# Optimization experiments

Hardware: AMD Instinct MI355X
Metric: run time of the kernel (lower is better)

## Reference

```python
import jax, jax.numpy as jnp
import numpy as np
from jax import lax

SUB_NO = 20; T_NO = 200; BASIS_NO = 19; T_DATA = 100000; E_NO = 800; I_NO = 200


def make_cos_basis():
    # raised-cosine log-time basis, [BASIS_NO, T_NO]
    i = jnp.arange(BASIS_NO, dtype=jnp.float32)[:, None]
    phi = (jnp.pi / 2.0) * i
    x = jnp.arange(T_NO, dtype=jnp.float32)[None, :]
    raw = 5.0 * jnp.log(x + 1.0)  # cos_scale=5, cos_shift=1
    basis = 0.5 * jnp.cos(raw - phi) + 0.5
    return jnp.where((raw >= phi - jnp.pi) & (raw <= phi + jnp.pi), basis, 0.0)


def causal_group_conv(x, kern):
    # x: [T, sub], kern: [sub, T_no]; out[t,k] = sum_j kern[k,j]*x[t-j,k]
    xr = x.T[None]  # [1, sub, T]
    w = jnp.flip(kern, 1)[:, None, :]  # [sub, 1, T_no]
    out = lax.conv_general_dilated(xr, w, (1,), [(T_NO - 1, 0)],
                                   dimension_numbers=('NCH', 'OIH', 'NCH'),
                                   feature_group_count=kern.shape[0])
    return out[0].T  # [T, sub]


def hist_conv(z, kern):
    # matches torch: pad T_no leading zeros, valid corr with flipped kernel, drop last
    zp = jnp.concatenate([jnp.zeros((T_NO,), z.dtype), z])[None, None, :]
    w = jnp.flip(kern)[None, None, :]
    out = lax.conv_general_dilated(zp, w, (1,), 'VALID',
                                   dimension_numbers=('NCH', 'OIH', 'NCH'))
    return out[0, 0, :-1]  # [T]


def setup_inputs() -> dict:
    key = jax.random.key(0)
    ks = jax.random.split(key, 12)
    # binary dendritic tree: parent of node j is (j-1)//2; C_den[p, j] = 1
    parent = np.maximum((np.arange(SUB_NO) - 1) // 2, 0)
    C_den = np.zeros((SUB_NO, SUB_NO), np.float32)
    for j in range(1, SUB_NO):
        C_den[parent[j], j] = 1.0
    assign_e = jax.random.randint(ks[0], (E_NO,), 0, SUB_NO)
    assign_i = jax.random.randint(ks[1], (I_NO,), 0, SUB_NO)
    C_syn_e = jax.nn.one_hot(assign_e, SUB_NO, dtype=jnp.float32).T
    C_syn_i = jax.nn.one_hot(assign_i, SUB_NO, dtype=jnp.float32).T
    S_e = (jax.random.uniform(ks[2], (T_DATA, E_NO)) < 0.05).astype(jnp.float32)
    S_i = (jax.random.uniform(ks[3], (T_DATA, I_NO)) < 0.05).astype(jnp.float32)
    Z = (jax.random.uniform(ks[4], (T_DATA,)) < 0.02).astype(jnp.float32)
    return {
        'S_e': S_e, 'S_i': S_i, 'Z': Z,
        'C_den': jnp.asarray(C_den), 'C_syn_e': C_syn_e, 'C_syn_i': C_syn_i,
        'W_syn_ns': 0.1 * jax.random.normal(ks[5], (SUB_NO, BASIS_NO, 2)),
        'W_syn_s': 0.1 * jax.random.normal(ks[6], (SUB_NO, BASIS_NO, 2)),
        'W_sub_ns': 0.1 * jnp.ones((SUB_NO,), jnp.float32),
        'W_sub_s': 0.1 * jnp.ones((SUB_NO,), jnp.float32),
        'V_o': jax.random.normal(ks[7], (1,)),
        'Theta_ns': 0.1 * jax.random.normal(ks[8], (SUB_NO,)),
        'Theta_s': 0.1 * jax.random.normal(ks[9], (SUB_NO,)),
        'hist_s_weights': 0.1 * jax.random.normal(ks[10], (BASIS_NO,)),
        'hist_ns_weights': 0.1 * jax.random.normal(ks[11], (BASIS_NO,)),
    }


def reference(S_e, S_i, Z, C_den, C_syn_e, C_syn_i, W_syn_ns, W_syn_s,
              W_sub_ns, W_sub_s, V_o, Theta_ns, Theta_s,
              hist_s_weights, hist_ns_weights):
    cb = make_cos_basis()
    syn_e = S_e @ C_syn_e.T  # [T, sub]
    syn_i = S_i @ C_syn_i.T
    e_kern_ns = W_syn_ns[:, :, 0] @ cb  # [sub, T_no]
    i_kern_ns = W_syn_ns[:, :, 1] @ cb
    e_kern_s = W_syn_s[:, :, 0] @ cb
    i_kern_s = W_syn_s[:, :, 1] @ cb
    syn_ns = causal_group_conv(syn_e, e_kern_ns) + causal_group_conv(syn_i, i_kern_ns)
    syn_s = causal_group_conv(syn_e, e_kern_s) + causal_group_conv(syn_i, i_kern_s)
    ws2 = W_sub_s ** 2
    wns2 = W_sub_ns ** 2
    T = S_e.shape[0]
    s_out = jnp.zeros((T, SUB_NO), syn_s.dtype)
    ns_out = jnp.zeros((T, SUB_NO), syn_ns.dtype)
    # leaf-to-root tree message passing; C_den[k] masks children of node k
    for k in range(SUB_NO - 1, 0, -1):
        mask = C_den[k]
        s_out = s_out.at[:, k].set(jnp.tanh(syn_s[:, k] + s_out @ (mask * ws2) + Theta_s[k]))
        ns_out = ns_out.at[:, k].set(jnp.tanh(syn_ns[:, k] + ns_out @ (mask * wns2) + Theta_ns[k]))
    hist_s_kern = hist_s_weights @ cb  # [T_no]
    hist_ns_kern = hist_ns_weights @ cb
    root_mask = C_den[0]
    final_Z = jax.nn.sigmoid(hist_conv(Z, hist_s_kern) + syn_s[:, 0]
                             + s_out @ (root_mask * ws2) + Theta_s[0])
    root_ns = jnp.tanh(hist_conv(Z, hist_ns_kern) + syn_ns[:, 0]
                       + ns_out @ (root_mask * wns2) + Theta_ns[0])
    final_V = root_ns * wns2[0] + V_o[0]
    out_filters = jnp.vstack([e_kern_ns, i_kern_ns, e_kern_s, i_kern_s,
                              hist_ns_kern[None], hist_s_kern[None]])
    return final_V, final_Z, out_filters
```

## Files before the change

### kernel.cpp

```cpp
#include <hip/hip_runtime.h>
#include <hip/hip_bf16.h>
#include <math.h>

#define SUB_NO 20
#define T_NO   200
#define BASIS_NO 19
#define T_DATA 100000
#define E_NO   800
#define I_NO   200

using u16 = unsigned short;
using u32 = unsigned int;
using u64 = unsigned long long;

__device__ __forceinline__ float bf2f(u16 h) {
  return __builtin_bit_cast(float, (u32)h << 16);
}
__device__ __forceinline__ u16 f2bf(float f) {
  u32 u = __builtin_bit_cast(u32, f);
  u += 0x7FFFu + ((u >> 16) & 1u);
  return (u16)(u >> 16);
}
__device__ __forceinline__ float ldx(const void* p, int i, bool bf) {
  return bf ? bf2f(((const u16*)p)[i]) : ((const float*)p)[i];
}
__device__ __forceinline__ void stx(void* p, int i, float v, bool bf) {
  if (bf) ((u16*)p)[i] = f2bf(v); else ((float*)p)[i] = v;
}

#define K0_BLOCKS 21
__global__ __launch_bounds__(256) void k0_prep(
    const u32* __restrict__ probe,
    const void* __restrict__ Wns, const void* __restrict__ Ws,
    const void* __restrict__ hsw, const void* __restrict__ hnsw,
    const void* __restrict__ Cse, const void* __restrict__ Csi,
    float* __restrict__ kern4, float* __restrict__ hist_s,
    float* __restrict__ hist_ns, int* __restrict__ ae, int* __restrict__ ai,
    void* __restrict__ out) {
  const bool bf = (probe[0] != 0u);
  __shared__ float cb[BASIS_NO * T_NO];
  const int tid = threadIdx.x;
  constexpr float PI = 3.14159265358979323846f;
  for (int idx = tid; idx < BASIS_NO * T_NO; idx += 256) {
    int b = idx / T_NO, j = idx - b * T_NO;
    float phi = 0.5f * PI * (float)b;
    float raw = 5.0f * logf((float)j + 1.0f);
    float v = 0.f;
    if (raw >= phi - PI && raw <= phi + PI) v = 0.5f * cosf(raw - phi) + 0.5f;
    cb[idx] = v;
  }
  __syncthreads();
  const int fbase = 2 * T_DATA;
  for (int gid = blockIdx.x * 256 + tid; gid < 5200; gid += K0_BLOCKS * 256) {
    if (gid < 4000) {
      int k = gid / T_NO, j = gid - k * T_NO;
      float e_ns = 0.f, i_ns = 0.f, e_s = 0.f, i_s = 0.f;
#pragma unroll
      for (int b = 0; b < BASIS_NO; ++b) {
        float c = cb[b * T_NO + j];
        e_ns = fmaf(ldx(Wns, (k * BASIS_NO + b) * 2 + 0, bf), c, e_ns);
        i_ns = fmaf(ldx(Wns, (k * BASIS_NO + b) * 2 + 1, bf), c, i_ns);
        e_s  = fmaf(ldx(Ws,  (k * BASIS_NO + b) * 2 + 0, bf), c, e_s);
        i_s  = fmaf(ldx(Ws,  (k * BASIS_NO + b) * 2 + 1, bf), c, i_s);
      }
      float* kp = kern4 + (j * SUB_NO + k) * 4;
      kp[0] = e_ns; kp[1] = i_ns; kp[2] = e_s; kp[3] = i_s;
      stx(out, fbase + (0 * SUB_NO + k) * T_NO + j, e_ns, bf);
      stx(out, fbase + (1 * SUB_NO + k) * T_NO + j, i_ns, bf);
      stx(out, fbase + (2 * SUB_NO + k) * T_NO + j, e_s,  bf);
      stx(out, fbase + (3 * SUB_NO + k) * T_NO + j, i_s,  bf);
    } else if (gid < 4200) {
      int j = gid - 4000;
      float hs = 0.f, hns = 0.f;
#pragma unroll
      for (int b = 0; b < BASIS_NO; ++b) {
        float c = cb[b * T_NO + j];
        hs  = fmaf(ldx(hsw,  b, bf), c, hs);
        hns = fmaf(ldx(hnsw, b, bf), c, hns);
      }
      hist_s[j] = hs; hist_ns[j] = hns;
      stx(out, fbase + 80 * T_NO + j, hns, bf);
      stx(out, fbase + 81 * T_NO + j, hs,  bf);
    } else if (gid < 5000) {
      int e = gid - 4200;
      int a = 0;
      for (int k = 0; k < SUB_NO; ++k) if (ldx(Cse, k * E_NO + e, bf) != 0.f) a = k;
      ae[e] = a;
    } else {
      int e = gid - 5000;
      int a = 0;
      for (int k = 0; k < SUB_NO; ++k) if (ldx(Csi, k * I_NO + e, bf) != 0.f) a = k;
      ai[e] = a;
    }
  }
}

#define K1_R 128

__global__ __launch_bounds__(256) void k1_agg(
    const u32* __restrict__ probe,
    const void* __restrict__ Se, const void* __restrict__ Si,
    const int* __restrict__ ae, const int* __restrict__ ai,
    u32* __restrict__ syn_pair) {
  const bool bf = (probe[0] != 0u);
  __shared__ u64 mask_e[SUB_NO][16];
  __shared__ u64 mask_i[SUB_NO][8];
  __shared__ int lae[E_NO];
  __shared__ int lai[I_NO];
  const int tid = threadIdx.x;
  const int l = tid & 63;
  const int wv = tid >> 6;
  for (int n = tid; n < E_NO; n += 256) lae[n] = ae[n];
  for (int n = tid; n < I_NO; n += 256) lai[n] = ai[n];
  __syncthreads();
  for (int pid = tid; pid < 480; pid += 256) {
    if (pid < 320) {
      int k = pid >> 4, w = pid & 15;
      u64 m = 0;
      if (bf) {
        if (w < 8) { for (int b = 0; b < 64; ++b) if (lae[8 * b + w] == k) m |= 1ull << b; }
        else       { for (int b = 0; b < 36; ++b) if (lae[512 + 8 * b + (w - 8)] == k) m |= 1ull << b; }
      } else {
        int g = w >> 2, j = w & 3;
        int lim = (g < 3) ? 64 : 8;
        for (int b = 0; b < lim; ++b) if (lae[256 * g + 4 * b + j] == k) m |= 1ull << b;
      }
      mask_e[k][w] = m;
    } else {
      int p2 = pid - 320; int k = p2 >> 3, w = p2 & 7;
      u64 m = 0;
      if (bf) { for (int b = 0; b < 25; ++b) { int e = 8 * b + w; if (e < I_NO && lai[e] == k) m |= 1ull << b; } }
      else if (w < 4) { for (int b = 0; b < 50; ++b) if (lai[4 * b + w] == k) m |= 1ull << b; }
      mask_i[k][w] = m;
    }
  }
  __syncthreads();
  u64 rme[16], rmi[8];
  const int ke = (l < SUB_NO) ? l : 0;
  const int ki = (l >= 32 && l < 32 + SUB_NO) ? l - 32 : 0;
#pragma unroll
  for (int w = 0; w < 16; ++w) rme[w] = mask_e[ke][w];
#pragma unroll
  for (int w = 0; w < 8; ++w) rmi[w] = mask_i[ki][w];

  const int r0 = blockIdx.x * K1_R + wv * 32;
  int nrows = T_DATA - r0; if (nrows > 32) nrows = 32;
  if (nrows <= 0) return;
  const uint4 z4 = make_uint4(0u, 0u, 0u, 0u);

  if (bf) {
    uint4 a0, a1, c0;
    {
      const uint4* p = (const uint4*)((const u16*)Se + (size_t)r0 * E_NO);
      a0 = p[l]; a1 = (l < 36) ? p[64 + l] : z4;
      const uint4* pi = (const uint4*)((const u16*)Si + (size_t)r0 * I_NO);
      c0 = (l < 25) ? pi[l] : z4;
    }
    for (int i = 0; i < nrows; ++i) {
      const int t = r0 + i;
      uint4 b0 = z4, b1 = z4, d0 = z4;
      if (i + 1 < nrows) {
        const uint4* p = (const uint4*)((const u16*)Se + (size_t)(t + 1) * E_NO);
        b0 = p[l]; b1 = (l < 36) ? p[64 + l] : z4;
        const uint4* pi = (const uint4*)((const u16*)Si + (size_t)(t + 1) * I_NO);
        d0 = (l < 25) ? pi[l] : z4;
      }
      u32 ce = 0, ci = 0;
#pragma unroll
      for (int j = 0; j < 8; ++j) {
        u32 d = (&a0.x)[j >> 1];
        u32 h = (j & 1) ? (d >> 16) : (d & 0xFFFFu);
        u64 m = __ballot(h != 0u);
        ce += (u32)__popcll(rme[j] & m);
      }
#pragma unroll
      for (int j = 0; j < 8; ++j) {
        u32 d = (&a1.x)[j >> 1];
        u32 h = (j & 1) ? (d >> 16) : (d & 0xFFFFu);
        u64 m = __ballot(h != 0u);
        ce += (u32)__popcll(rme[8 + j] & m);
      }
#pragma unroll
      for (int j = 0; j < 8; ++j) {
        u32 d = (&c0.x)[j >> 1];
        u32 h = (j & 1) ? (d >> 16) : (d & 0xFFFFu);
        u64 m = __ballot(h != 0u);
        ci += (u32)__popcll(rmi[j] & m);
      }
      u32 pe = (u32)f2bf((float)ce);
      u32 pif = (u32)f2bf((float)ci);
      u32 other = __shfl(pif, (l + 32) & 63, 64);
      if (l < SUB_NO) syn_pair[(size_t)t * SUB_NO + l] = pe | (other << 16);
      a0 = b0; a1 = b1; c0 = d0;
    }
  } else {
    uint4 a0, a1, a2, a3, c0;
    {
      const uint4* p = (const uint4*)((const float*)Se + (size_t)r0 * E_NO);
      a0 = p[l]; a1 = p[64 + l]; a2 = p[128 + l]; a3 = (l < 8) ? p[192 + l] : z4;
      const uint4* pi = (const uint4*)((const float*)Si + (size_t)r0 * I_NO);
      c0 = (l < 50) ? pi[l] : z4;
    }
    for (int i = 0; i < nrows; ++i) {
      const int t = r0 + i;
      uint4 b0 = z4, b1 = z4, b2 = z4, b3 = z4, d0 = z4;
      if (i + 1 < nrows) {
        const uint4* p = (const uint4*)((const float*)Se + (size_t)(t + 1) * E_NO);
        b0 = p[l]; b1 = p[64 + l]; b2 = p[128 + l]; b3 = (l < 8) ? p[192 + l] : z4;
        const uint4* pi = (const uint4*)((const float*)Si + (size_t)(t + 1) * I_NO);
        d0 = (l < 50) ? pi[l] : z4;
      }
      u32 ce = 0, ci = 0;
      const uint4 va[4] = {a0, a1, a2, a3};
#pragma unroll
      for (int g = 0; g < 4; ++g) {
#pragma unroll
        for (int j = 0; j < 4; ++j) {
          u32 d = (&va[g].x)[j];
          u64 m = __ballot(d != 0u);
          ce += (u32)__popcll(rme[4 * g + j] & m);
        }
      }
#pragma unroll
      for (int j = 0; j < 4; ++j) {
        u32 d = (&c0.x)[j];
        u64 m = __ballot(d != 0u);
        ci += (u32)__popcll(rmi[j] & m);
      }
      u32 pe = (u32)f2bf((float)ce);
      u32 pif = (u32)f2bf((float)ci);
      u32 other = __shfl(pif, (l + 32) & 63, 64);
      if (l < SUB_NO) syn_pair[(size_t)t * SUB_NO + l] = pe | (other << 16);
      a0 = b0; a1 = b1; a2 = b2; a3 = b3; c0 = d0;
    }
  }
}

#define K2T  64
#define K2R  (K2T + T_NO)
#define K2CH 40

__global__ __launch_bounds__(320) void k2_conv(
    const u32* __restrict__ probe,
    const u32* __restrict__ syn_pair, const float* __restrict__ kern4,
    const float* __restrict__ hist_s, const float* __restrict__ hist_ns,
    const void* __restrict__ Z, const void* __restrict__ Wsub_ns,
    const void* __restrict__ Wsub_s, const void* __restrict__ Vo,
    const void* __restrict__ Thns, const void* __restrict__ Ths,
    void* __restrict__ out) {
  const bool bf = (probe[0] != 0u);
  __shared__ uint4 tile4[K2R * 5];
  __shared__ float4 kc4[K2CH * SUB_NO];
  __shared__ float accsh[K2T][42];
  __shared__ float hps[5][K2T], hpns[5][K2T];
  __shared__ float ztile[K2R];
  __shared__ float lhs[T_NO], lhns[T_NO];
  __shared__ float ws2_l[SUB_NO], wns2_l[SUB_NO], ths_l[SUB_NO], thns_l[SUB_NO];
  const int tid = threadIdx.x;
  const int l = tid & 63;
  const int kg = tid >> 6;
  const int t0 = blockIdx.x * K2T;

  const int base4 = (t0 - T_NO) * (SUB_NO / 4);
  const uint4* sp4 = (const uint4*)syn_pair;
  for (int n = tid; n < K2R * 5; n += 320) {
    int g = base4 + n;
    uint4 v = make_uint4(0u, 0u, 0u, 0u);
    if (g >= 0 && g < T_DATA * SUB_NO / 4) v = sp4[g];
    tile4[n] = v;
  }
  const int zbase = t0 - T_NO;
  for (int n = tid; n < K2R; n += 320) {
    int g = zbase + n;
    ztile[n] = (g >= 0 && g < T_DATA) ? ldx(Z, g, bf) : 0.f;
  }
  for (int n = tid; n < T_NO; n += 320) { lhs[n] = hist_s[n]; lhns[n] = hist_ns[n]; }
  if (tid < SUB_NO) {
    float w = ldx(Wsub_s, tid, bf);   ws2_l[tid]  = w * w;
    float wn = ldx(Wsub_ns, tid, bf); wns2_l[tid] = wn * wn;
    ths_l[tid]  = ldx(Ths, tid, bf);
    thns_l[tid] = ldx(Thns, tid, bf);
  }
  __syncthreads();

  float a_ns[4] = {0.f, 0.f, 0.f, 0.f};
  float a_s[4]  = {0.f, 0.f, 0.f, 0.f};
  float hsa = 0.f, hnsa = 0.f;
  const int mlo = 40 * kg;

  for (int ch = 0; ch < T_NO / K2CH; ++ch) {
    const float4* ksrc = (const float4*)(kern4 + ch * K2CH * SUB_NO * 4);
    for (int n = tid; n < K2CH * SUB_NO; n += 320) kc4[n] = ksrc[n];
    __syncthreads();
#pragma unroll 2
    for (int mm = 0; mm < K2CH; ++mm) {
      const int m = ch * K2CH + mm;
      uint4 q = tile4[(l + T_NO - m) * 5 + kg];
      if ((unsigned)(m - mlo) < 40u) {
        float zv = ztile[l + T_NO - 1 - m];
        hsa  = fmaf(lhs[m],  zv, hsa);
        hnsa = fmaf(lhns[m], zv, hnsa);
      }
      const float4* kp = &kc4[mm * SUB_NO + kg * 4];
      float4 c0 = kp[0], c1 = kp[1], c2 = kp[2], c3 = kp[3];
      float ev0 = __builtin_bit_cast(float, q.x << 16);
      float iv0 = __builtin_bit_cast(float, q.x & 0xFFFF0000u);
      float ev1 = __builtin_bit_cast(float, q.y << 16);
      float iv1 = __builtin_bit_cast(float, q.y & 0xFFFF0000u);
      float ev2 = __builtin_bit_cast(float, q.z << 16);
      float iv2 = __builtin_bit_cast(float, q.z & 0xFFFF0000u);
      float ev3 = __builtin_bit_cast(float, q.w << 16);
      float iv3 = __builtin_bit_cast(float, q.w & 0xFFFF0000u);
      a_ns[0] = fmaf(c0.x, ev0, a_ns[0]); a_ns[0] = fmaf(c0.y, iv0, a_ns[0]);
      a_s[0]  = fmaf(c0.z, ev0, a_s[0]);  a_s[0]  = fmaf(c0.w, iv0, a_s[0]);
      a_ns[1] = fmaf(c1.x, ev1, a_ns[1]); a_ns[1] = fmaf(c1.y, iv1, a_ns[1]);
      a_s[1]  = fmaf(c1.z, ev1, a_s[1]);  a_s[1]  = fmaf(c1.w, iv1, a_s[1]);
      a_ns[2] = fmaf(c2.x, ev2, a_ns[2]); a_ns[2] = fmaf(c2.y, iv2, a_ns[2]);
      a_s[2]  = fmaf(c2.z, ev2, a_s[2]);  a_s[2]  = fmaf(c2.w, iv2, a_s[2]);
      a_ns[3] = fmaf(c3.x, ev3, a_ns[3]); a_ns[3] = fmaf(c3.y, iv3, a_ns[3]);
      a_s[3]  = fmaf(c3.z, ev3, a_s[3]);  a_s[3]  = fmaf(c3.w, iv3, a_s[3]);
    }
    __syncthreads();
  }

  hps[kg][l] = hsa; hpns[kg][l] = hnsa;
#pragma unroll
  for (int j = 0; j < 4; ++j) {
    accsh[l][kg * 4 + j]      = a_s[j];
    accsh[l][21 + kg * 4 + j] = a_ns[j];
  }
  __syncthreads();

  if (kg == 0) {
    float h_s  = hps[0][l] + hps[1][l] + hps[2][l] + hps[3][l] + hps[4][l];
    float h_ns = hpns[0][l] + hpns[1][l] + hpns[2][l] + hpns[3][l] + hpns[4][l];
    float so[SUB_NO], no[SUB_NO];
#pragma unroll
    for (int k = SUB_NO - 1; k >= 1; --k) {
      float as_ = accsh[l][k] + ths_l[k];
      float an_ = accsh[l][21 + k] + thns_l[k];
      const int c1 = 2 * k + 1, c2 = 2 * k + 2;
      if (c1 < SUB_NO) { as_ += ws2_l[c1] * so[c1]; an_ += wns2_l[c1] * no[c1]; }
      if (c2 < SUB_NO) { as_ += ws2_l[c2] * so[c2]; an_ += wns2_l[c2] * no[c2]; }
      so[k] = tanhf(as_);
      no[k] = tanhf(an_);
    }
    float zs = h_s + accsh[l][0] + ths_l[0] + ws2_l[1] * so[1] + ws2_l[2] * so[2];
    float zn = h_ns + accsh[l][21] + thns_l[0] + wns2_l[1] * no[1] + wns2_l[2] * no[2];
    float fZ = 1.f / (1.f + expf(-zs));
    float fV = tanhf(zn) * wns2_l[0] + ldx(Vo, 0, bf);
    const int t = t0 + l;
    if (t < T_DATA) {
      stx(out, t, fV, bf);
      stx(out, T_DATA + t, fZ, bf);
    }
  }
}

extern "C" void kernel_launch(void* const* d_in, const int* in_sizes, int n_in,
                              void* d_out, int out_size, void* d_ws, size_t ws_size,
                              hipStream_t stream) {
  const void* Se      = d_in[0];
  const void* Si      = d_in[1];
  const void* Z       = d_in[2];
  const u32*  probe   = (const u32*)d_in[3];
  const void* Cse     = d_in[4];
  const void* Csi     = d_in[5];
  const void* Wns     = d_in[6];
  const void* Ws_     = d_in[7];
  const void* Wsub_ns = d_in[8];
  const void* Wsub_s  = d_in[9];
  const void* Vo      = d_in[10];
  const void* Thns    = d_in[11];
  const void* Ths     = d_in[12];
  const void* hsw     = d_in[13];
  const void* hnsw    = d_in[14];

  float* wsf      = (float*)d_ws;
  float* kern4    = wsf;
  float* hist_s   = wsf + 16000;
  float* hist_ns  = wsf + 16200;
  int*   ae       = (int*)(wsf + 16400);
  int*   ai       = (int*)(wsf + 17200);
  u32*   syn_pair = (u32*)(wsf + 17408);

  hipLaunchKernelGGL(k0_prep, dim3(K0_BLOCKS), dim3(256), 0, stream,
                     probe, Wns, Ws_, hsw, hnsw, Cse, Csi,
                     kern4, hist_s, hist_ns, ae, ai, d_out);
  hipLaunchKernelGGL(k1_agg, dim3((T_DATA + K1_R - 1) / K1_R), dim3(256), 0, stream,
                     probe, Se, Si, ae, ai, syn_pair);
  hipLaunchKernelGGL(k2_conv, dim3((T_DATA + K2T - 1) / K2T), dim3(320), 0, stream,
                     probe, syn_pair, kern4, hist_s, hist_ns, Z,
                     Wsub_ns, Wsub_s, Vo, Thns, Ths, d_out);
}
```

Before: 705.2 us.

## Register-block conv over two time rows and alias shared tile buffers

The convolution kernel now computes two time positions per thread (128 rows per block), so each kernel coefficient loaded from LDS is reused twice. Kernel coefficients are reordered so accumulators pair as float2. The syn tile and the reduction scratch share one aliased shared buffer to keep LDS usage low enough for a 5-wave occupancy hint, and the chunk size is halved. The aggregation kernel gets smaller row tiles (16 rows per wave), which launches more blocks. The trade-offs are higher register pressure and a finalisation phase that now runs on two waves.

After: 648.8 us. 8.0% less time.

```diff
diff --git a/kernel.cpp b/kernel.cpp
--- a/kernel.cpp
+++ b/kernel.cpp
@@ -64,7 +64,7 @@
         i_s  = fmaf(ldx(Ws,  (k * BASIS_NO + b) * 2 + 1, bf), c, i_s);
       }
       float* kp = kern4 + (j * SUB_NO + k) * 4;
-      kp[0] = e_ns; kp[1] = i_ns; kp[2] = e_s; kp[3] = i_s;
+      kp[0] = e_ns; kp[1] = e_s; kp[2] = i_ns; kp[3] = i_s;
       stx(out, fbase + (0 * SUB_NO + k) * T_NO + j, e_ns, bf);
       stx(out, fbase + (1 * SUB_NO + k) * T_NO + j, i_ns, bf);
       stx(out, fbase + (2 * SUB_NO + k) * T_NO + j, e_s,  bf);
@@ -95,7 +95,7 @@
   }
 }
 
-#define K1_R 128
+#define K1_R 64
 
 __global__ __launch_bounds__(256) void k1_agg(
     const u32* __restrict__ probe,
@@ -143,8 +143,8 @@
 #pragma unroll
   for (int w = 0; w < 8; ++w) rmi[w] = mask_i[ki][w];
 
-  const int r0 = blockIdx.x * K1_R + wv * 32;
-  int nrows = T_DATA - r0; if (nrows > 32) nrows = 32;
+  const int r0 = blockIdx.x * K1_R + wv * 16;
+  int nrows = T_DATA - r0; if (nrows > 16) nrows = 16;
   if (nrows <= 0) return;
   const uint4 z4 = make_uint4(0u, 0u, 0u, 0u);
 
@@ -236,11 +236,11 @@
   }
 }
 
-#define K2T  64
+#define K2T  128
 #define K2R  (K2T + T_NO)
-#define K2CH 40
-
-__global__ __launch_bounds__(320) void k2_conv(
+#define K2CH 20
+
+__global__ __launch_bounds__(320, 5) void k2_conv(
     const u32* __restrict__ probe,
     const u32* __restrict__ syn_pair, const float* __restrict__ kern4,
     const float* __restrict__ hist_s, const float* __restrict__ hist_ns,
@@ -249,10 +249,11 @@
     const void* __restrict__ Thns, const void* __restrict__ Ths,
     void* __restrict__ out) {
   const bool bf = (probe[0] != 0u);
-  __shared__ uint4 tile4[K2R * 5];
+  __shared__ __align__(16) unsigned char smem[K2R * SUB_NO * 4];
+  uint4* tile4 = (uint4*)smem;
+  float* accsh = (float*)smem;
+  float* hp    = (float*)(smem + 21000);
   __shared__ float4 kc4[K2CH * SUB_NO];
-  __shared__ float accsh[K2T][42];
-  __shared__ float hps[5][K2T], hpns[5][K2T];
   __shared__ float ztile[K2R];
   __shared__ float lhs[T_NO], lhns[T_NO];
   __shared__ float ws2_l[SUB_NO], wns2_l[SUB_NO], ths_l[SUB_NO], thns_l[SUB_NO];
@@ -283,9 +284,13 @@
   }
   __syncthreads();
 
-  float a_ns[4] = {0.f, 0.f, 0.f, 0.f};
-  float a_s[4]  = {0.f, 0.f, 0.f, 0.f};
-  float hsa = 0.f, hnsa = 0.f;
+  float2 acc_a[4], acc_b[4];
+#pragma unroll
+  for (int j = 0; j < 4; ++j) {
+    acc_a[j] = make_float2(0.f, 0.f);
+    acc_b[j] = make_float2(0.f, 0.f);
+  }
+  float hs_a = 0.f, hns_a = 0.f, hs_b = 0.f, hns_b = 0.f;
   const int mlo = 40 * kg;
 
   for (int ch = 0; ch < T_NO / K2CH; ++ch) {
@@ -295,61 +300,73 @@
 #pragma unroll 2
     for (int mm = 0; mm < K2CH; ++mm) {
       const int m = ch * K2CH + mm;
-      uint4 q = tile4[(l + T_NO - m) * 5 + kg];
+      uint4 qa = tile4[(l + T_NO - m) * 5 + kg];
+      uint4 qb = tile4[(l + 64 + T_NO - m) * 5 + kg];
       if ((unsigned)(m - mlo) < 40u) {
-        float zv = ztile[l + T_NO - 1 - m];
-        hsa  = fmaf(lhs[m],  zv, hsa);
-        hnsa = fmaf(lhns[m], zv, hnsa);
+        float ls = lhs[m], lns = lhns[m];
+        float za = ztile[l + T_NO - 1 - m];
+        float zb = ztile[l + 64 + T_NO - 1 - m];
+        hs_a = fmaf(ls, za, hs_a);   hns_a = fmaf(lns, za, hns_a);
+        hs_b = fmaf(ls, zb, hs_b);   hns_b = fmaf(lns, zb, hns_b);
       }
       const float4* kp = &kc4[mm * SUB_NO + kg * 4];
-      float4 c0 = kp[0], c1 = kp[1], c2 = kp[2], c3 = kp[3];
-      float ev0 = __builtin_bit_cast(float, q.x << 16);
-      float iv0 = __builtin_bit_cast(float, q.x & 0xFFFF0000u);
-      float ev1 = __builtin_bit_cast(float, q.y << 16);
-      float iv1 = __builtin_bit_cast(float, q.y & 0xFFFF0000u);
-      float ev2 = __builtin_bit_cast(float, q.z << 16);
-      float iv2 = __builtin_bit_cast(float, q.z & 0xFFFF0000u);
-      float ev3 = __builtin_bit_cast(float, q.w << 16);
-      float iv3 = __builtin_bit_cast(float, q.w & 0xFFFF0000u);
-      a_ns[0] = fmaf(c0.x, ev0, a_ns[0]); a_ns[0] = fmaf(c0.y, iv0, a_ns[0]);
-      a_s[0]  = fmaf(c0.z, ev0, a_s[0]);  a_s[0]  = fmaf(c0.w, iv0, a_s[0]);
-      a_ns[1] = fmaf(c1.x, ev1, a_ns[1]); a_ns[1] = fmaf(c1.y, iv1, a_ns[1]);
-      a_s[1]  = fmaf(c1.z, ev1, a_s[1]);  a_s[1]  = fmaf(c1.w, iv1, a_s[1]);
-      a_ns[2] = fmaf(c2.x, ev2, a_ns[2]); a_ns[2] = fmaf(c2.y, iv2, a_ns[2]);
-      a_s[2]  = fmaf(c2.z, ev2, a_s[2]);  a_s[2]  = fmaf(c2.w, iv2, a_s[2]);
-      a_ns[3] = fmaf(c3.x, ev3, a_ns[3]); a_ns[3] = fmaf(c3.y, iv3, a_ns[3]);
-      a_s[3]  = fmaf(c3.z, ev3, a_s[3]);  a_s[3]  = fmaf(c3.w, iv3, a_s[3]);
+#pragma unroll
+      for (int j = 0; j < 4; ++j) {
+        float4 c = kp[j];
+        u32 ua = (&qa.x)[j], ub = (&qb.x)[j];
+        float ea = __builtin_bit_cast(float, ua << 16);
+        float ia = __builtin_bit_cast(float, ua & 0xFFFF0000u);
+        float eb = __builtin_bit_cast(float, ub << 16);
+        float ib = __builtin_bit_cast(float, ub & 0xFFFF0000u);
+        acc_a[j].x = fmaf(c.x, ea, acc_a[j].x);
+        acc_a[j].y = fmaf(c.y, ea, acc_a[j].y);
+        acc_a[j].x = fmaf(c.z, ia, acc_a[j].x);
+        acc_a[j].y = fmaf(c.w, ia, acc_a[j].y);
+        acc_b[j].x = fmaf(c.x, eb, acc_b[j].x);
+        acc_b[j].y = fmaf(c.y, eb, acc_b[j].y);
+        acc_b[j].x = fmaf(c.z, ib, acc_b[j].x);
+        acc_b[j].y = fmaf(c.w, ib, acc_b[j].y);
+      }
     }
     __syncthreads();
   }
 
-  hps[kg][l] = hsa; hpns[kg][l] = hnsa;
 #pragma unroll
   for (int j = 0; j < 4; ++j) {
-    accsh[l][kg * 4 + j]      = a_s[j];
-    accsh[l][21 + kg * 4 + j] = a_ns[j];
-  }
+    const int k = kg * 4 + j;
+    accsh[l * 41 + k]            = acc_a[j].y;
+    accsh[l * 41 + 20 + k]       = acc_a[j].x;
+    accsh[(l + 64) * 41 + k]      = acc_b[j].y;
+    accsh[(l + 64) * 41 + 20 + k] = acc_b[j].x;
+  }
+  float* hp_s = hp;
+  float* hp_ns = hp + 640;
+  hp_s[kg * 128 + l] = hs_a;  hp_s[kg * 128 + 64 + l] = hs_b;
+  hp_ns[kg * 128 + l] = hns_a; hp_ns[kg * 128 + 64 + l] = hns_b;
   __syncthreads();
 
-  if (kg == 0) {
-    float h_s  = hps[0][l] + hps[1][l] + hps[2][l] + hps[3][l] + hps[4][l];
-    float h_ns = hpns[0][l] + hpns[1][l] + hpns[2][l] + hpns[3][l] + hpns[4][l];
+  if (kg < 2) {
+    const int tl = kg * 64 + l;
+    float h_s = 0.f, h_ns = 0.f;
+#pragma unroll
+    for (int w = 0; w < 5; ++w) { h_s += hp_s[w * 128 + tl]; h_ns += hp_ns[w * 128 + tl]; }
+    const float* ar = &accsh[tl * 41];
     float so[SUB_NO], no[SUB_NO];
 #pragma unroll
     for (int k = SUB_NO - 1; k >= 1; --k) {
-      float as_ = accsh[l][k] + ths_l[k];
-      float an_ = accsh[l][21 + k] + thns_l[k];
+      float as_ = ar[k] + ths_l[k];
+      float an_ = ar[20 + k] + thns_l[k];
       const int c1 = 2 * k + 1, c2 = 2 * k + 2;
       if (c1 < SUB_NO) { as_ += ws2_l[c1] * so[c1]; an_ += wns2_l[c1] * no[c1]; }
       if (c2 < SUB_NO) { as_ += ws2_l[c2] * so[c2]; an_ += wns2_l[c2] * no[c2]; }
       so[k] = tanhf(as_);
       no[k] = tanhf(an_);
     }
-    float zs = h_s + accsh[l][0] + ths_l[0] + ws2_l[1] * so[1] + ws2_l[2] * so[2];
-    float zn = h_ns + accsh[l][21] + thns_l[0] + wns2_l[1] * no[1] + wns2_l[2] * no[2];
+    float zs = h_s + ar[0] + ths_l[0] + ws2_l[1] * so[1] + ws2_l[2] * so[2];
+    float zn = h_ns + ar[20] + thns_l[0] + wns2_l[1] * no[1] + wns2_l[2] * no[2];
     float fZ = 1.f / (1.f + expf(-zs));
     float fV = tanhf(zn) * wns2_l[0] + ldx(Vo, 0, bf);
-    const int t = t0 + l;
+    const int t = t0 + tl;
     if (t < T_DATA) {
       stx(out, t, fV, bf);
       stx(out, T_DATA + t, fZ, bf);
```
